# Performance work log

Hardware: AMD Instinct MI355X
Metric: run time of the kernel (lower is better)

## Reference

```python
import jax, jax.numpy as jnp
import numpy as np

B, N, E, C = 2, 10000, 150000, 256
EPS = 1e-5  # torch BatchNorm1d default eps


def _bn(x, gamma, beta):
    # BatchNorm1d in training mode: biased batch statistics over the row dim.
    m = x.mean(axis=0)
    v = x.var(axis=0)
    return (x - m) * jax.lax.rsqrt(v + EPS) * gamma + beta


def setup_inputs() -> dict:
    key = jax.random.key(0)
    ks = jax.random.split(key, 6)
    xyz = jax.random.normal(ks[0], (B, N, 3), jnp.float32)
    features = jax.random.normal(ks[1], (B, C, N), jnp.float32)
    edges = jax.random.randint(ks[2], (B, 2, E), 0, N, jnp.int32)
    W_e = jax.random.normal(ks[3], (C + 3, C), jnp.float32) * 0.02
    b_e = jnp.zeros((C,), jnp.float32)
    g_e = jnp.ones((C,), jnp.float32)
    beta_e = jnp.zeros((C,), jnp.float32)
    W_u = jax.random.normal(ks[4], (C, C), jnp.float32) * 0.02
    b_u = jnp.zeros((C,), jnp.float32)
    g_u = jnp.ones((C,), jnp.float32)
    beta_u = jnp.zeros((C,), jnp.float32)
    return {"xyz": xyz, "features": features, "edges": edges,
            "W_e": W_e, "b_e": b_e, "g_e": g_e, "beta_e": beta_e,
            "W_u": W_u, "b_u": b_u, "g_u": g_u, "beta_u": beta_u}


def reference(xyz, features, edges, W_e, b_e, g_e, beta_e, W_u, b_u, g_u, beta_u):
    vf = jnp.transpose(features, (0, 2, 1))        # [B, N, C]
    ed = jnp.transpose(edges, (0, 2, 1))           # [B, E, 2]
    src, dst = ed[..., 0], ed[..., 1]              # [B, E]
    gather = jax.vmap(lambda v, i: v[i])
    s_feat = gather(vf, src)                       # [B, E, C]
    s_xyz = gather(xyz, src)                       # [B, E, 3]
    d_xyz = gather(xyz, dst)                       # [B, E, 3]
    ef = jnp.concatenate([s_feat, s_xyz - d_xyz], axis=-1).reshape(-1, C + 3)
    h = _bn(jax.nn.relu(ef @ W_e + b_e), g_e, beta_e).reshape(B, E, C)
    # scatter-max by destination vertex
    agg = jax.vmap(lambda f, i: jax.ops.segment_max(f, i, num_segments=N))(h, dst)
    agg = jnp.where(jnp.isfinite(agg), agg, 0.0)   # empty segments -> 0 (torch_scatter fill)
    u = _bn(jax.nn.relu(agg.reshape(-1, C) @ W_u + b_u), g_u, beta_u).reshape(B, N, C)
    out = u + vf                                   # residual
    return jnp.transpose(out, (0, 2, 1))           # [B, C, N]
```

## Files before the change

kernel.cpp:

```cpp
#include <hip/hip_runtime.h>

#define B_ 2
#define N_ 10000
#define E_ 150000
#define C_ 256
#define M_EDGE (B_*E_)
#define M_NODE (B_*N_)
#define ED_CAP (M_EDGE + 3*M_NODE + 64)
#define NW_ 4096
#define SPAN_CAP 256
#define EPS_ 1e-5f

typedef unsigned short u16;
typedef unsigned int   u32;
typedef unsigned long long u64;
typedef __attribute__((ext_vector_type(8))) __bf16 bf16x8;
typedef __attribute__((ext_vector_type(4))) float  f32x4;
typedef _Float16 h2 __attribute__((ext_vector_type(2)));

__device__ __forceinline__ u16 f2bf(float x) {
  union { float f; u32 u; } v; v.f = x;
  u32 r = v.u + 0x7FFFu + ((v.u >> 16) & 1u);
  return (u16)(r >> 16);
}
__device__ __forceinline__ float bf2f(u16 x) {
  union { u32 u; float f; } v; v.u = ((u32)x) << 16; return v.f;
}
__device__ __forceinline__ u16 f2h(float x) {
  _Float16 h = (_Float16)x;
  union { _Float16 h; u16 u; } v; v.h = h; return v.u;
}
__device__ __forceinline__ float h2f(u32 bits) {
  union { u16 u; _Float16 h; } v; v.u = (u16)bits; return (float)v.h;
}
__device__ __forceinline__ h2 u2h2(u32 x) {
  union { u32 u; h2 h; } v; v.u = x; return v.h;
}
__device__ __forceinline__ u32 h22u(h2 x) {
  union { h2 h; u32 u; } v; v.h = x; return v.u;
}

__device__ __forceinline__ void async16(void* lds, const void* g) {
  __builtin_amdgcn_global_load_lds(
      (const __attribute__((address_space(1))) void*)g,
      (__attribute__((address_space(3))) void*)lds, 16, 0, 0);
}

__device__ __forceinline__ u32 zload(const u16* zp, u32 si) {
  u32 r;
  u64 a = (u64)(zp + ((size_t)si << 8));
  asm volatile("global_load_dword %0, %1, off" : "=v"(r) : "v"(a) : "memory");
  return r;
}

__global__ void k_init(int* __restrict__ counts, float* __restrict__ stats) {
  int i = blockIdx.x * 256 + threadIdx.x;
  if (i < M_NODE) counts[i] = 0;
  if (i < 1024) stats[i] = 0.f;
}

__global__ void k_transpose_feat(const float* __restrict__ f, u16* __restrict__ vf) {
  __shared__ float tile[32][33];
  int tx = threadIdx.x & 31, ty = threadIdx.x >> 5;
  int b = blockIdx.z, c0 = blockIdx.y * 32, n0 = blockIdx.x * 32;
  #pragma unroll
  for (int i = 0; i < 4; i++) {
    int c = c0 + ty + i*8, n = n0 + tx;
    tile[ty + i*8][tx] = (n < N_) ? f[((size_t)(b*C_ + c))*N_ + n] : 0.f;
  }
  __syncthreads();
  #pragma unroll
  for (int i = 0; i < 4; i++) {
    int n = n0 + ty + i*8, c = c0 + tx;
    if (n < N_) vf[((size_t)(b*N_ + n))*C_ + c] = f2bf(tile[tx][ty + i*8]);
  }
}

__global__ void k_transpose_w(const float* __restrict__ We, const float* __restrict__ Wu,
                              u16* __restrict__ WeT, u16* __restrict__ WuT) {
  __shared__ float tile[32][33];
  const float* src = blockIdx.z ? Wu : We;
  u16* dst = blockIdx.z ? WuT : WeT;
  int tx = threadIdx.x & 31, ty = threadIdx.x >> 5;
  int r0 = blockIdx.y * 32, c0 = blockIdx.x * 32;
  #pragma unroll
  for (int i = 0; i < 4; i++)
    tile[ty + i*8][tx] = src[(size_t)(r0 + ty + i*8)*C_ + c0 + tx];
  __syncthreads();
  #pragma unroll
  for (int i = 0; i < 4; i++)
    dst[(size_t)(c0 + ty + i*8)*C_ + r0 + tx] = f2bf(tile[tx][ty + i*8]);
}

__global__ void k_hist(const int* __restrict__ edges, int* __restrict__ counts) {
  int i = blockIdx.x * 256 + threadIdx.x;
  if (i >= M_EDGE) return;
  int b = (i >= E_) ? 1 : 0;
  int e = i - b * E_;
  int d = edges[(size_t)(b*2 + 1)*E_ + e];
  atomicAdd(&counts[b*N_ + d], 1);
}

__global__ __launch_bounds__(1024)
void k_scan(const int* __restrict__ counts, int* __restrict__ offs, int* __restrict__ cursor) {
  __shared__ int part[1024];
  int t = threadIdx.x;
  int base = t * 20;
  int vals[20];
  if (t < 1000) {
    #pragma unroll
    for (int j = 0; j < 5; j++)
      *(int4*)&vals[j*4] = *(const int4*)&counts[base + j*4];
  } else {
    #pragma unroll
    for (int i = 0; i < 20; i++) vals[i] = 0;
  }
  int local[20];
  int s = 0;
  #pragma unroll
  for (int i = 0; i < 20; i++) {
    int pv = (vals[i] + 3) & ~3;
    local[i] = s; s += pv;
  }
  part[t] = s;
  __syncthreads();
  for (int d = 1; d < 1024; d <<= 1) {
    int v = (t >= d) ? part[t - d] : 0;
    __syncthreads();
    part[t] += v;
    __syncthreads();
  }
  int excl = (t == 0) ? 0 : part[t - 1];
  if (t < 1000) {
    #pragma unroll
    for (int j = 0; j < 5; j++) {
      int4 o;
      o.x = excl + local[j*4 + 0];
      o.y = excl + local[j*4 + 1];
      o.z = excl + local[j*4 + 2];
      o.w = excl + local[j*4 + 3];
      *(int4*)&offs[base + j*4]   = o;
      *(int4*)&cursor[base + j*4] = o;
    }
  }
  if (t == 1023) offs[M_NODE] = part[1023];
}

__global__ void k_scatter(const int* __restrict__ edges, const float* __restrict__ xyz,
                          int* __restrict__ cursor, uint2* __restrict__ ed) {
  int i = blockIdx.x * 256 + threadIdx.x;
  if (i >= M_EDGE) return;
  int b = (i >= E_) ? 1 : 0;
  int e = i - b * E_;
  int s = edges[(size_t)(b*2 + 0)*E_ + e];
  int d = edges[(size_t)(b*2 + 1)*E_ + e];
  const float* ps = xyz + ((size_t)(b*N_ + s))*3;
  const float* pd = xyz + ((size_t)(b*N_ + d))*3;
  int pos = atomicAdd(&cursor[b*N_ + d], 1);
  u32 rx = (u32)f2h(ps[0]-pd[0]) | ((u32)f2h(ps[1]-pd[1]) << 16);
  u32 ry = (u32)f2h(ps[2]-pd[2]) | ((u32)(b*N_ + s) << 16);
  ed[pos] = make_uint2(rx, ry);
}

__global__ void k_pad(const int* __restrict__ offs, const int* __restrict__ counts,
                      uint2* __restrict__ ed, u32* __restrict__ nodeInfo,
                      int* __restrict__ waveStart) {
  int i = blockIdx.x * 256 + threadIdx.x;
  const int T = offs[M_NODE];
  const int SPW = (T + NW_ - 1) / NW_;
  if (i < M_NODE) {
    int s = offs[i], e = offs[i+1];
    int cnt = counts[i];
    if (cnt > 0) {
      int pad = e - (s + cnt);
      if (pad) {
        uint2 f = ed[s];
        for (int k = 0; k < pad; k++) ed[s + cnt + k] = f;
      }
    }
    nodeInfo[i] = ((u32)e << 10) | (u32)cnt;
    int lo = (i == 0) ? 0 : offs[i-1] + 1;
    int wlo = (lo + SPW - 1) / SPW;
    int whi = offs[i] / SPW;
    for (int w = wlo; w <= whi && w <= NW_; w++) waveStart[w] = i;
  }
  if (i == M_NODE) {
    nodeInfo[M_NODE]   = ((u32)T << 10);
    nodeInfo[M_NODE+1] = ((u32)T << 10);
    int lo = offs[M_NODE-1] + 1;
    int wlo = (lo + SPW - 1) / SPW;
    if (wlo < 0) wlo = 0;
    for (int w = wlo; w <= NW_; w++) waveStart[w] = M_NODE;
  }
  int pos = T + i;
  if (pos < ED_CAP) ed[pos] = make_uint2(0u, 0u);
}

__global__ __launch_bounds__(256)
void k_zgemm(const u16* __restrict__ A, const u16* __restrict__ WeT,
             const float* __restrict__ be, u16* __restrict__ zh)
{
  __shared__ __align__(16) u16 As[128*32];
  __shared__ __align__(16) u16 Bs[128*32];
  const int t  = threadIdx.x;
  const int n0 = blockIdx.x * 128;
  const int mb = blockIdx.y * 128;

  int r0 = mb + (t >> 2);      if (r0 >= M_NODE) r0 = 0;
  int r1 = mb + 64 + (t >> 2); if (r1 >= M_NODE) r1 = 0;
  const int ak = (((t & 3) ^ ((t >> 3) & 3)) << 3);
  const u16* asrc0 = A + (size_t)r0 * C_ + ak;
  const u16* asrc1 = A + (size_t)r1 * C_ + ak;
  const u16* bsrc0 = WeT + (size_t)(n0 + (t >> 2)) * C_ + ak;
  const u16* bsrc1 = WeT + (size_t)(n0 + 64 + (t >> 2)) * C_ + ak;

  const f32x4 zero = {0.f, 0.f, 0.f, 0.f};
  f32x4 acc[4][4];
  #pragma unroll
  for (int m = 0; m < 4; m++)
    #pragma unroll
    for (int n = 0; n < 4; n++) acc[m][n] = zero;

  const int lane = t & 63, wave = t >> 6;
  const int wr = wave >> 1, wc = wave & 1;
  const int lr = lane & 15, lch = lane >> 4;
  const int swz = (lr >> 1) & 3;

  for (int kk = 0; kk < 8; kk++) {
    const int k0 = kk * 32;
    async16(&As[t*8],        asrc0 + k0);
    async16(&As[(t+256)*8],  asrc1 + k0);
    async16(&Bs[t*8],        bsrc0 + k0);
    async16(&Bs[(t+256)*8],  bsrc1 + k0);
    __syncthreads();
    bf16x8 a[4], b[4];
    #pragma unroll
    for (int m = 0; m < 4; m++)
      a[m] = *(const bf16x8*)&As[(wr*64 + m*16 + lr)*32 + ((lch ^ swz) << 3)];
    #pragma unroll
    for (int n = 0; n < 4; n++)
      b[n] = *(const bf16x8*)&Bs[(wc*64 + n*16 + lr)*32 + ((lch ^ swz) << 3)];
    #pragma unroll
    for (int m = 0; m < 4; m++)
      #pragma unroll
      for (int n = 0; n < 4; n++)
        acc[m][n] = __builtin_amdgcn_mfma_f32_16x16x32_bf16(a[m], b[n], acc[m][n], 0, 0, 0);
    __syncthreads();
  }

  int gc[4]; float bias[4];
  #pragma unroll
  for (int n = 0; n < 4; n++) { int c = n0 + wc*64 + n*16 + lr; gc[n] = c; bias[n] = be[c]; }
  #pragma unroll
  for (int m = 0; m < 4; m++) {
    #pragma unroll
    for (int j = 0; j < 4; j++) {
      int r = mb + wr*64 + m*16 + lch*4 + j;
      if (r < M_NODE) {
        #pragma unroll
        for (int n = 0; n < 4; n++)
          zh[(size_t)r * C_ + gc[n]] = f2h(acc[m][n][j] + bias[n]);
      }
    }
  }
}

__global__ __launch_bounds__(512)
void k_agg(const u16* __restrict__ zh, const uint2* __restrict__ ed,
           const int* __restrict__ offs, const u32* __restrict__ nodeInfo,
           const int* __restrict__ waveStart,
           const float* __restrict__ We, const float* __restrict__ ge,
           u32* __restrict__ aggh, float* __restrict__ esum, float* __restrict__ esumsq)
{
  __shared__ __align__(16) uint2 rec[8][SPAN_CAP];
  __shared__ float red[8][128];

  const int tid  = threadIdx.x;
  const int lane = tid & 63;
  const int wave = __builtin_amdgcn_readfirstlane(tid >> 6);
  const int grp  = __builtin_amdgcn_readfirstlane(blockIdx.x & 1);
  const int c0   = grp * 128 + lane * 2;
  const h2 w0 = h2{(_Float16)We[256*C_ + c0], (_Float16)We[256*C_ + c0 + 1]};
  const h2 w1 = h2{(_Float16)We[257*C_ + c0], (_Float16)We[257*C_ + c0 + 1]};
  const h2 w2 = h2{(_Float16)We[258*C_ + c0], (_Float16)We[258*C_ + c0 + 1]};
  const float ge0 = ge[c0], ge1 = ge[c0 + 1];
  const u16* zp = zh + c0;

  const h2 hzero = h2{(_Float16)0.f, (_Float16)0.f};
  const h2 MXI = h2{(_Float16)-1.f, (_Float16)-1.f};
  const h2 MNI = h2{(_Float16)65504.f, (_Float16)65504.f};
  h2 psh = hzero, pqh = hzero;

  const int wid  = (blockIdx.x >> 1) * 8 + wave;
  int cur        = __builtin_amdgcn_readfirstlane(waveStart[wid]);
  const int nEnd = __builtin_amdgcn_readfirstlane(waveStart[wid + 1]);

  if (cur < nEnd) {
    const int uBeg = __builtin_amdgcn_readfirstlane(offs[cur]);
    const int uEnd = __builtin_amdgcn_readfirstlane(offs[nEnd]);
    const int span = uEnd - uBeg;
    if (span > 0) {
      for (int s = lane; s < span; s += 64) rec[wave][s] = ed[uBeg + s];

      u32 info = nodeInfo[cur];
      while ((int)(info >> 10) == uBeg) { cur++; info = nodeInfo[cur]; }
      int curEnd   = (int)(info >> 10);
      int vE       = uBeg + (int)(info & 1023u);
      u32 nextInfo = nodeInfo[cur + 1];

      h2 mx = MXI, mn = MNI;
      const int nc = span >> 2;
      u32 Z[4][4];

      auto flushNode = [&]() {
        h2 s;
        s.x = (ge0 >= 0.f) ? mx.x : mn.x;
        s.y = (ge1 >= 0.f) ? mx.y : mn.y;
        aggh[(size_t)cur * 128 + grp * 64 + lane] = h22u(s);
      };

#define ISSUEZ(ZB, CI) { \
      int _c = (CI) < nc - 1 ? (CI) : nc - 1; \
      uint4 _a = *(const uint4*)&rec[wave][_c*4]; \
      uint4 _b = *(const uint4*)&rec[wave][_c*4 + 2]; \
      Z[ZB][0] = zload(zp, _a.y >> 16); \
      Z[ZB][1] = zload(zp, _a.w >> 16); \
      Z[ZB][2] = zload(zp, _b.y >> 16); \
      Z[ZB][3] = zload(zp, _b.w >> 16); }

#define PROCSLOT(RX, RY, ZV, KOFF) { \
      h2 dxx = u2h2(((RX) & 0xffffu) | ((RX) << 16)); \
      h2 dyy = u2h2(((RX) >> 16) | ((RX) & 0xffff0000u)); \
      h2 dzz = u2h2(((RY) & 0xffffu) | ((RY) << 16)); \
      h2 y = dxx*w0 + dyy*w1 + dzz*w2 + u2h2(ZV); \
      y = __builtin_elementwise_max(y, hzero); \
      mx = __builtin_elementwise_max(mx, y); \
      mn = __builtin_elementwise_min(mn, y); \
      if (slot + (KOFF) < vE) { psh = psh + y; pqh = y*y + pqh; } }

#define PHASE(J, ZW, ZR) { \
      uint4 rA = *(const uint4*)&rec[wave][(J)*4]; \
      uint4 rB = *(const uint4*)&rec[wave][(J)*4 + 2]; \
      ISSUEZ(ZW, (J) + 3) \
      asm volatile("s_waitcnt vmcnt(12)" ::: "memory"); \
      __builtin_amdgcn_sched_barrier(0); \
      const int slot = uBeg + (J)*4; \
      if (slot == curEnd) { \
        flushNode(); \
        mx = MXI; mn = MNI; \
        cur++; \
        u32 inf = nextInfo; \
        while ((int)(inf >> 10) == curEnd) { cur++; inf = nodeInfo[cur]; } \
        vE = curEnd + (int)(inf & 1023u); \
        curEnd = (int)(inf >> 10); \
        nextInfo = nodeInfo[cur + 1]; \
      } \
      PROCSLOT(rA.x, rA.y, Z[ZR][0], 0) \
      PROCSLOT(rA.z, rA.w, Z[ZR][1], 1) \
      PROCSLOT(rB.x, rB.y, Z[ZR][2], 2) \
      PROCSLOT(rB.z, rB.w, Z[ZR][3], 3) }

      ISSUEZ(0, 0) ISSUEZ(1, 1) ISSUEZ(2, 2)

      for (int j = 0; j < nc; j += 4) {
        PHASE(j + 0, 3, 0)
        if (j + 1 < nc) PHASE(j + 1, 0, 1)
        if (j + 2 < nc) PHASE(j + 2, 1, 2)
        if (j + 3 < nc) PHASE(j + 3, 2, 3)
      }
      flushNode();
#undef ISSUEZ
#undef PROCSLOT
#undef PHASE
    }
  }

  float ps0 = (float)psh.x, ps1 = (float)psh.y;
  float pq0 = (float)pqh.x, pq1 = (float)pqh.y;
  red[wave][lane*2]     = ps0;
  red[wave][lane*2 + 1] = ps1;
  __syncthreads();
  if (tid < 128) {
    float s = 0.f;
    #pragma unroll
    for (int w = 0; w < 8; w++) s += red[w][tid];
    atomicAdd(&esum[grp*128 + tid], s);
  }
  __syncthreads();
  red[wave][lane*2]     = pq0;
  red[wave][lane*2 + 1] = pq1;
  __syncthreads();
  if (tid < 128) {
    float s = 0.f;
    #pragma unroll
    for (int w = 0; w < 8; w++) s += red[w][tid];
    atomicAdd(&esumsq[grp*128 + tid], s);
  }
}

__global__ void k_stats(const float* __restrict__ sum, const float* __restrict__ sumsq,
                        const float* __restrict__ g, const float* __restrict__ beta,
                        float cnt, float* __restrict__ scale, float* __restrict__ shift) {
  int c = threadIdx.x;
  float m = sum[c] / cnt;
  float v = sumsq[c] / cnt - m*m;
  v = fmaxf(v, 0.f);
  float s = g[c] * rsqrtf(v + EPS_);
  scale[c] = s;
  shift[c] = beta[c] - m*s;
}

__global__ void k_aggnorm(const u32* __restrict__ aggh, const int* __restrict__ counts,
                          const float* __restrict__ scale, const float* __restrict__ shift,
                          u32* __restrict__ out) {
  int i = blockIdx.x * 256 + threadIdx.x;
  if (i >= M_NODE*C_/2) return;
  int n = i >> 7;
  int p = (i & 127) * 2;
  int cnt = counts[n];
  u32 hv = aggh[i];
  float v0 = (cnt > 0) ? fmaf(h2f(hv & 0xffffu), scale[p],   shift[p])   : 0.f;
  float v1 = (cnt > 0) ? fmaf(h2f(hv >> 16),     scale[p+1], shift[p+1]) : 0.f;
  out[i] = ((u32)f2bf(v0)) | (((u32)f2bf(v1)) << 16);
}

__global__ __launch_bounds__(256)
void k_ugemm(const u16* __restrict__ A, const u16* __restrict__ WuT,
             const float* __restrict__ bu,
             u16* __restrict__ yu, float* __restrict__ usum, float* __restrict__ usumsq)
{
  __shared__ __align__(16) u16 As[128*32];
  __shared__ __align__(16) u16 Bs[128*32];
  const int t  = threadIdx.x;
  const int n0 = blockIdx.x * 128;
  const int mb = blockIdx.y * 128;

  int r0 = mb + (t >> 2);      if (r0 >= M_NODE) r0 = 0;
  int r1 = mb + 64 + (t >> 2); if (r1 >= M_NODE) r1 = 0;
  const int ak = (((t & 3) ^ ((t >> 3) & 3)) << 3);
  const u16* asrc0 = A + (size_t)r0 * C_ + ak;
  const u16* asrc1 = A + (size_t)r1 * C_ + ak;
  const u16* bsrc0 = WuT + (size_t)(n0 + (t >> 2)) * C_ + ak;
  const u16* bsrc1 = WuT + (size_t)(n0 + 64 + (t >> 2)) * C_ + ak;

  const f32x4 zero = {0.f, 0.f, 0.f, 0.f};
  f32x4 acc[4][4];
  #pragma unroll
  for (int m = 0; m < 4; m++)
    #pragma unroll
    for (int n = 0; n < 4; n++) acc[m][n] = zero;

  const int lane = t & 63, wave = t >> 6;
  const int wr = wave >> 1, wc = wave & 1;
  const int lr = lane & 15, lch = lane >> 4;
  const int swz = (lr >> 1) & 3;

  for (int kk = 0; kk < 8; kk++) {
    const int k0 = kk * 32;
    async16(&As[t*8],        asrc0 + k0);
    async16(&As[(t+256)*8],  asrc1 + k0);
    async16(&Bs[t*8],        bsrc0 + k0);
    async16(&Bs[(t+256)*8],  bsrc1 + k0);
    __syncthreads();
    bf16x8 a[4], b[4];
    #pragma unroll
    for (int m = 0; m < 4; m++)
      a[m] = *(const bf16x8*)&As[(wr*64 + m*16 + lr)*32 + ((lch ^ swz) << 3)];
    #pragma unroll
    for (int n = 0; n < 4; n++)
      b[n] = *(const bf16x8*)&Bs[(wc*64 + n*16 + lr)*32 + ((lch ^ swz) << 3)];
    #pragma unroll
    for (int m = 0; m < 4; m++)
      #pragma unroll
      for (int n = 0; n < 4; n++)
        acc[m][n] = __builtin_amdgcn_mfma_f32_16x16x32_bf16(a[m], b[n], acc[m][n], 0, 0, 0);
    __syncthreads();
  }

  int gc[4]; float bias[4];
  #pragma unroll
  for (int n = 0; n < 4; n++) { int c = n0 + wc*64 + n*16 + lr; gc[n] = c; bias[n] = bu[c]; }
  float psum[4] = {0.f,0.f,0.f,0.f};
  float psq [4] = {0.f,0.f,0.f,0.f};
  #pragma unroll
  for (int m = 0; m < 4; m++) {
    #pragma unroll
    for (int j = 0; j < 4; j++) {
      int r = mb + wr*64 + m*16 + lch*4 + j;
      bool valid = r < M_NODE;
      #pragma unroll
      for (int n = 0; n < 4; n++) {
        float y = fmaxf(acc[m][n][j] + bias[n], 0.f);
        if (valid) {
          psum[n] += y;
          psq[n]  += y*y;
          yu[(size_t)r * C_ + gc[n]] = f2bf(y);
        }
      }
    }
  }
  #pragma unroll
  for (int n = 0; n < 4; n++) {
    float s1 = psum[n], s2 = psq[n];
    s1 += __shfl_xor(s1, 16, 64);  s2 += __shfl_xor(s2, 16, 64);
    s1 += __shfl_xor(s1, 32, 64);  s2 += __shfl_xor(s2, 32, 64);
    if (lch == 0) { atomicAdd(&usum[gc[n]], s1); atomicAdd(&usumsq[gc[n]], s2); }
  }
}

__global__ void k_final(const u16* __restrict__ yu, const u16* __restrict__ vf,
                        const float* __restrict__ scale, const float* __restrict__ shift,
                        float* __restrict__ out) {
  __shared__ float tile[32][33];
  int tx = threadIdx.x & 31, ty = threadIdx.x >> 5;
  int b = blockIdx.z, c0 = blockIdx.y * 32, n0 = blockIdx.x * 32;
  #pragma unroll
  for (int i = 0; i < 4; i++) {
    int n = n0 + ty + i*8, c = c0 + tx;
    float v = 0.f;
    if (n < N_) {
      size_t idx = ((size_t)(b*N_ + n))*C_ + c;
      v = bf2f(yu[idx]) * scale[c] + shift[c] + bf2f(vf[idx]);
    }
    tile[ty + i*8][tx] = v;
  }
  __syncthreads();
  int n = n0 + tx;
  if (n < N_) {
    #pragma unroll
    for (int i = 0; i < 4; i++) {
      int c = c0 + ty + i*8;
      out[((size_t)(b*C_ + c))*N_ + n] = tile[tx][ty + i*8];
    }
  }
}

extern "C" void kernel_launch(void* const* d_in, const int* in_sizes, int n_in,
                              void* d_out, int out_size, void* d_ws, size_t ws_size,
                              hipStream_t stream) {
  const float* xyz  = (const float*)d_in[0];
  const float* feat = (const float*)d_in[1];
  const int*   edges= (const int*)  d_in[2];
  const float* We   = (const float*)d_in[3];
  const float* be   = (const float*)d_in[4];
  const float* ge   = (const float*)d_in[5];
  const float* bte  = (const float*)d_in[6];
  const float* Wu   = (const float*)d_in[7];
  const float* bu   = (const float*)d_in[8];
  const float* gu   = (const float*)d_in[9];
  const float* btu  = (const float*)d_in[10];
  float* out = (float*)d_out;

  char* w = (char*)d_ws;
  size_t off = 0;
  auto carve = [&](size_t bytes) -> void* {
    void* p = w + off;
    off = (off + bytes + 511) & ~(size_t)511;
    return p;
  };
  u16*  vf       = (u16*) carve((size_t)M_NODE*C_*2);
  u16*  WeT      = (u16*) carve((size_t)C_*C_*2);
  u16*  WuT      = (u16*) carve((size_t)C_*C_*2);
  u16*  zh       = (u16*) carve((size_t)M_NODE*C_*2);
  uint2* ed      = (uint2*)carve((size_t)ED_CAP*8);
  int*  counts   = (int*) carve((size_t)M_NODE*4);
  int*  offs     = (int*) carve((size_t)(M_NODE+1)*4);
  int*  cursor   = (int*) carve((size_t)M_NODE*4);
  u32*  nodeInfo = (u32*) carve((size_t)(M_NODE+2)*4);
  int*  waveStart= (int*) carve((size_t)(NW_+1)*4);
  u32*  aggh     = (u32*) carve((size_t)M_NODE*128*4);
  u32*  aggnorm  = (u32*) carve((size_t)M_NODE*C_*2);
  u16*  yu       = (u16*) carve((size_t)M_NODE*C_*2);
  float* stats   = (float*)carve(2048*4);
  float* esum = stats,        *esumsq = stats + 256;
  float* usum = stats + 512,  *usumsq = stats + 768;
  float* scale_e = stats + 1024, *shift_e = stats + 1280;
  float* scale_u = stats + 1536, *shift_u = stats + 1792;

  k_init<<<dim3((M_NODE + 255)/256), 256, 0, stream>>>(counts, stats);
  k_transpose_feat<<<dim3((N_+31)/32, C_/32, B_), 256, 0, stream>>>(feat, vf);
  k_transpose_w<<<dim3(C_/32, C_/32, 2), 256, 0, stream>>>(We, Wu, WeT, WuT);
  k_hist<<<dim3((M_EDGE + 255)/256), 256, 0, stream>>>(edges, counts);
  k_scan<<<1, 1024, 0, stream>>>(counts, offs, cursor);
  k_scatter<<<dim3((M_EDGE + 255)/256), 256, 0, stream>>>(edges, xyz, cursor, ed);
  k_pad<<<dim3((M_NODE + 255)/256), 256, 0, stream>>>(offs, counts, ed, nodeInfo, waveStart);
  k_zgemm<<<dim3(2, (M_NODE + 127)/128), 256, 0, stream>>>(vf, WeT, be, zh);
  k_agg<<<dim3(NW_/8*2), 512, 0, stream>>>(zh, ed, offs, nodeInfo, waveStart,
                                           We, ge, aggh, esum, esumsq);
  k_stats<<<1, 256, 0, stream>>>(esum, esumsq, ge, bte, (float)M_EDGE, scale_e, shift_e);
  k_aggnorm<<<dim3(M_NODE*C_/512), 256, 0, stream>>>(aggh, counts, scale_e, shift_e, aggnorm);
  k_ugemm<<<dim3(2, (M_NODE + 127)/128), 256, 0, stream>>>(
      (const u16*)aggnorm, WuT, bu, yu, usum, usumsq);
  k_stats<<<1, 256, 0, stream>>>(usum, usumsq, gu, btu, (float)M_NODE, scale_u, shift_u);
  k_final<<<dim3((N_+31)/32, C_/32, B_), 256, 0, stream>>>(yu, vf, scale_u, shift_u, out);
}
```

Measured before the change: 156.4 us.

## Fuse aggregate normalization into u-GEMM and deepen gather prefetch in k_agg

The separate k_aggnorm pass, which applied the edge BatchNorm scale/shift and empty-segment zeroing and wrote a bf16 copy, is removed. k_ugemm now reads the fp16 max aggregates directly, normalizes them in registers with scale/shift staged in LDS, and stores bf16 into the A tile. This saves one kernel launch and a full write and re-read of the intermediate. Separately, the z-row gather pipeline in k_agg is deepened from 3 to 5 chunks ahead with an 8-slot register ring, which hides more gather latency but uses more VGPRs. The A loads in the GEMM become synchronous global loads instead of async copies, so they overlap less.

```diff
diff --git a/kernel.cpp b/kernel.cpp
--- a/kernel.cpp
+++ b/kernel.cpp
@@ -310,7 +310,7 @@
 
       h2 mx = MXI, mn = MNI;
       const int nc = span >> 2;
-      u32 Z[4][4];
+      u32 Z[8][4];
 
       auto flushNode = [&]() {
         h2 s;
@@ -341,8 +341,8 @@
 #define PHASE(J, ZW, ZR) { \
       uint4 rA = *(const uint4*)&rec[wave][(J)*4]; \
       uint4 rB = *(const uint4*)&rec[wave][(J)*4 + 2]; \
-      ISSUEZ(ZW, (J) + 3) \
-      asm volatile("s_waitcnt vmcnt(12)" ::: "memory"); \
+      ISSUEZ(ZW, (J) + 5) \
+      asm volatile("s_waitcnt vmcnt(20)" ::: "memory"); \
       __builtin_amdgcn_sched_barrier(0); \
       const int slot = uBeg + (J)*4; \
       if (slot == curEnd) { \
@@ -360,13 +360,17 @@
       PROCSLOT(rB.x, rB.y, Z[ZR][2], 2) \
       PROCSLOT(rB.z, rB.w, Z[ZR][3], 3) }
 
-      ISSUEZ(0, 0) ISSUEZ(1, 1) ISSUEZ(2, 2)
-
-      for (int j = 0; j < nc; j += 4) {
-        PHASE(j + 0, 3, 0)
-        if (j + 1 < nc) PHASE(j + 1, 0, 1)
-        if (j + 2 < nc) PHASE(j + 2, 1, 2)
-        if (j + 3 < nc) PHASE(j + 3, 2, 3)
+      ISSUEZ(0, 0) ISSUEZ(1, 1) ISSUEZ(2, 2) ISSUEZ(3, 3) ISSUEZ(4, 4)
+
+      for (int j = 0; j < nc; j += 8) {
+        PHASE(j + 0, 5, 0)
+        if (j + 1 < nc) PHASE(j + 1, 6, 1)
+        if (j + 2 < nc) PHASE(j + 2, 7, 2)
+        if (j + 3 < nc) PHASE(j + 3, 0, 3)
+        if (j + 4 < nc) PHASE(j + 4, 1, 4)
+        if (j + 5 < nc) PHASE(j + 5, 2, 5)
+        if (j + 6 < nc) PHASE(j + 6, 3, 6)
+        if (j + 7 < nc) PHASE(j + 7, 4, 7)
       }
       flushNode();
 #undef ISSUEZ
@@ -410,36 +414,29 @@
   shift[c] = beta[c] - m*s;
 }
 
-__global__ void k_aggnorm(const u32* __restrict__ aggh, const int* __restrict__ counts,
-                          const float* __restrict__ scale, const float* __restrict__ shift,
-                          u32* __restrict__ out) {
-  int i = blockIdx.x * 256 + threadIdx.x;
-  if (i >= M_NODE*C_/2) return;
-  int n = i >> 7;
-  int p = (i & 127) * 2;
-  int cnt = counts[n];
-  u32 hv = aggh[i];
-  float v0 = (cnt > 0) ? fmaf(h2f(hv & 0xffffu), scale[p],   shift[p])   : 0.f;
-  float v1 = (cnt > 0) ? fmaf(h2f(hv >> 16),     scale[p+1], shift[p+1]) : 0.f;
-  out[i] = ((u32)f2bf(v0)) | (((u32)f2bf(v1)) << 16);
-}
-
 __global__ __launch_bounds__(256)
-void k_ugemm(const u16* __restrict__ A, const u16* __restrict__ WuT,
-             const float* __restrict__ bu,
+void k_ugemm(const u32* __restrict__ aggh, const int* __restrict__ counts,
+             const float* __restrict__ scale_e, const float* __restrict__ shift_e,
+             const u16* __restrict__ WuT, const float* __restrict__ bu,
              u16* __restrict__ yu, float* __restrict__ usum, float* __restrict__ usumsq)
 {
   __shared__ __align__(16) u16 As[128*32];
   __shared__ __align__(16) u16 Bs[128*32];
+  __shared__ float sscale[256], sshift[256];
   const int t  = threadIdx.x;
   const int n0 = blockIdx.x * 128;
   const int mb = blockIdx.y * 128;
 
+  sscale[t] = scale_e[t];
+  sshift[t] = shift_e[t];
+
   int r0 = mb + (t >> 2);      if (r0 >= M_NODE) r0 = 0;
   int r1 = mb + 64 + (t >> 2); if (r1 >= M_NODE) r1 = 0;
   const int ak = (((t & 3) ^ ((t >> 3) & 3)) << 3);
-  const u16* asrc0 = A + (size_t)r0 * C_ + ak;
-  const u16* asrc1 = A + (size_t)r1 * C_ + ak;
+  const bool nz0 = counts[r0] > 0;
+  const bool nz1 = counts[r1] > 0;
+  const u32* ag0 = aggh + (size_t)r0 * 128 + (ak >> 1);
+  const u32* ag1 = aggh + (size_t)r1 * 128 + (ak >> 1);
   const u16* bsrc0 = WuT + (size_t)(n0 + (t >> 2)) * C_ + ak;
   const u16* bsrc1 = WuT + (size_t)(n0 + 64 + (t >> 2)) * C_ + ak;
 
@@ -455,10 +452,33 @@
   const int lr = lane & 15, lch = lane >> 4;
   const int swz = (lr >> 1) & 3;
 
+  __syncthreads();
+
   for (int kk = 0; kk < 8; kk++) {
     const int k0 = kk * 32;
-    async16(&As[t*8],        asrc0 + k0);
-    async16(&As[(t+256)*8],  asrc1 + k0);
+    uint4 a0 = *(const uint4*)(ag0 + (k0 >> 1));
+    uint4 a1 = *(const uint4*)(ag1 + (k0 >> 1));
+    const int base = k0 + ak;
+    float4 sc0 = *(const float4*)&sscale[base];
+    float4 sc1 = *(const float4*)&sscale[base + 4];
+    float4 sh0 = *(const float4*)&sshift[base];
+    float4 sh1 = *(const float4*)&sshift[base + 4];
+    auto cvt = [&](u32 q, float s0, float b0, float s1, float b1, bool nz) -> u32 {
+      float v0 = nz ? fmaf(h2f(q & 0xffffu), s0, b0) : 0.f;
+      float v1 = nz ? fmaf(h2f(q >> 16),     s1, b1) : 0.f;
+      return ((u32)f2bf(v0)) | (((u32)f2bf(v1)) << 16);
+    };
+    uint4 p0, p1;
+    p0.x = cvt(a0.x, sc0.x, sh0.x, sc0.y, sh0.y, nz0);
+    p0.y = cvt(a0.y, sc0.z, sh0.z, sc0.w, sh0.w, nz0);
+    p0.z = cvt(a0.z, sc1.x, sh1.x, sc1.y, sh1.y, nz0);
+    p0.w = cvt(a0.w, sc1.z, sh1.z, sc1.w, sh1.w, nz0);
+    p1.x = cvt(a1.x, sc0.x, sh0.x, sc0.y, sh0.y, nz1);
+    p1.y = cvt(a1.y, sc0.z, sh0.z, sc0.w, sh0.w, nz1);
+    p1.z = cvt(a1.z, sc1.x, sh1.x, sc1.y, sh1.y, nz1);
+    p1.w = cvt(a1.w, sc1.z, sh1.z, sc1.w, sh1.w, nz1);
+    *(uint4*)&As[t*8]       = p0;
+    *(uint4*)&As[(t+256)*8] = p1;
     async16(&Bs[t*8],        bsrc0 + k0);
     async16(&Bs[(t+256)*8],  bsrc1 + k0);
     __syncthreads();
@@ -569,7 +589,6 @@
   u32*  nodeInfo = (u32*) carve((size_t)(M_NODE+2)*4);
   int*  waveStart= (int*) carve((size_t)(NW_+1)*4);
   u32*  aggh     = (u32*) carve((size_t)M_NODE*128*4);
-  u32*  aggnorm  = (u32*) carve((size_t)M_NODE*C_*2);
   u16*  yu       = (u16*) carve((size_t)M_NODE*C_*2);
   float* stats   = (float*)carve(2048*4);
   float* esum = stats,        *esumsq = stats + 256;
@@ -588,9 +607,8 @@
   k_agg<<<dim3(NW_/8*2), 512, 0, stream>>>(zh, ed, offs, nodeInfo, waveStart,
                                            We, ge, aggh, esum, esumsq);
   k_stats<<<1, 256, 0, stream>>>(esum, esumsq, ge, bte, (float)M_EDGE, scale_e, shift_e);
-  k_aggnorm<<<dim3(M_NODE*C_/512), 256, 0, stream>>>(aggh, counts, scale_e, shift_e, aggnorm);
   k_ugemm<<<dim3(2, (M_NODE + 127)/128), 256, 0, stream>>>(
-      (const u16*)aggnorm, WuT, bu, yu, usum, usumsq);
+      aggh, counts, scale_e, shift_e, WuT, bu, yu, usum, usumsq);
   k_stats<<<1, 256, 0, stream>>>(usum, usumsq, gu, btu, (float)M_NODE, scale_u, shift_u);
   k_final<<<dim3((N_+31)/32, C_/32, B_), 256, 0, stream>>>(yu, vf, scale_u, shift_u, out);
 }
```

Measured after the change: 151.2 us. -3.3%, faster.
